# Performance work log

Hardware: AMD Instinct MI355X
Metric: run time of the kernel (lower is better)

## Reference

```python
import jax, jax.numpy as jnp
import numpy as np

N_NODES = 50000
N_NEIB = 64
D = 256
BATCH = 1024
N_SAMPLES = (25, 10)  # fanout per layer (layer_specs n_sample)


def setup_inputs() -> dict:
    key = jax.random.key(0)
    ks = jax.random.split(key, 12)
    inp = {
        'ids': jax.random.randint(ks[0], (BATCH,), 0, N_NODES),
        'diff_idx': jax.random.randint(ks[1], (N_NODES, N_NEIB), 0, N_NODES),
        'diff_val': jax.random.uniform(ks[2], (N_NODES, N_NEIB), dtype=jnp.float32),
        'feats': jax.random.normal(ks[3], (N_NODES, D), dtype=jnp.float32),
    }
    # two aggregator layers, each: fc_x, fc_neib : D -> D (= output_dim//2)
    for li in range(2):
        inp[f'Wx{li+1}'] = jax.random.normal(ks[4 + 4 * li], (D, D), dtype=jnp.float32) * 0.05
        inp[f'bx{li+1}'] = jnp.zeros((D,), dtype=jnp.float32)
        inp[f'Wn{li+1}'] = jax.random.normal(ks[5 + 4 * li], (D, D), dtype=jnp.float32) * 0.05
        inp[f'bn{li+1}'] = jnp.zeros((D,), dtype=jnp.float32)
    return inp


def _sample(diff_idx, diff_val, ids, n_samples, key):
    # gather candidate neighbor rows, shared random column permutation, take first n_samples
    tmp_idx = diff_idx[ids]            # [n, N_NEIB]
    tmp_val = diff_val[ids]
    perm = jax.random.permutation(key, tmp_idx.shape[1])
    idx = tmp_idx[:, perm][:, :n_samples].reshape(-1)
    val = tmp_val[:, perm][:, :n_samples].reshape(-1)
    return idx, val


def _agg(x, neib, vals, Wx, bx, Wn, bn):
    # weighted-mean neighbor aggregation + self/neib linear combine + relu
    n = x.shape[0]
    d = neib.shape[1]
    neib = neib.reshape(n, -1, d)              # [n, s, d]
    vals = vals.reshape(n, -1)                 # [n, s]
    w = vals / (jnp.sum(vals, axis=1, keepdims=True) + 1e-10)
    m = jnp.einsum('nsd,ns->nd', neib, w)      # weighted mean of neighbors
    return jax.nn.relu(x @ Wx + bx + m @ Wn + bn)


def reference(ids, diff_idx, diff_val, feats,
              Wx1, bx1, Wn1, bn1, Wx2, bx2, Wn2, bn2):
    skey = jax.random.key(42)
    all_feats = [feats[ids]]
    all_vals = []
    cur = ids
    for li, n in enumerate(N_SAMPLES):
        cur, vals = _sample(diff_idx, diff_val, cur, n, jax.random.fold_in(skey, li))
        all_feats.append(feats[cur])
        all_vals.append(vals)
    params = [(Wx1, bx1, Wn1, bn1), (Wx2, bx2, Wn2, bn2)]
    for Wx, bx, Wn, bn in params:
        all_feats = [_agg(all_feats[k], all_feats[k + 1], all_vals[k], Wx, bx, Wn, bn)
                     for k in range(len(all_feats) - 1)]
    assert len(all_feats) == 1
    return all_feats[0]  # [BATCH, D]
```

## Files before the change

### kernel.cpp

```cpp
#include <hip/hip_runtime.h>
#include <stdint.h>
#include <stddef.h>
#include <algorithm>

#define BATCH  1024
#define S1     25
#define S2     10
#define DIM    256
#define NNEIB  64
#define L2ROWS (BATCH * S1)
#define MROWS  (BATCH + BATCH * S1)
#define KTOT   512
#define NFEAT  50000

struct Perm25 { int p[S1]; };
struct Perm10 { int p[S2]; };

typedef __attribute__((ext_vector_type(8))) short short8;
typedef __attribute__((ext_vector_type(4))) float f32x4;

static inline uint32_t rotl_(uint32_t x, int d) { return (x << d) | (x >> (32 - d)); }

static void tf2x32(uint32_t k0, uint32_t k1, uint32_t x0, uint32_t x1,
                   uint32_t* o0, uint32_t* o1) {
  const uint32_t ks0 = k0, ks1 = k1, ks2 = k0 ^ k1 ^ 0x1BD11BDAu;
  static const int R[8] = {13, 15, 26, 6, 17, 29, 16, 24};
  x0 += ks0; x1 += ks1;
  for (int g = 0; g < 5; ++g) {
    const int* rr = R + (g & 1) * 4;
    for (int i = 0; i < 4; i++) { x0 += x1; x1 = rotl_(x1, rr[i]); x1 ^= x0; }
    uint32_t a, b;
    switch (g) {
      default:
      case 0: a = ks1; b = ks2; break;
      case 1: a = ks2; b = ks0; break;
      case 2: a = ks0; b = ks1; break;
      case 3: a = ks1; b = ks2; break;
      case 4: a = ks2; b = ks0; break;
    }
    x0 += a; x1 = x1 + b + (uint32_t)(g + 1);
  }
  *o0 = x0; *o1 = x1;
}

static void compute_perm(uint32_t li, int n, int* out) {
  uint32_t k0, k1, s0, s1;
  tf2x32(0u, 42u, 0u, li, &k0, &k1);
  tf2x32(k0, k1, 0u, 1u, &s0, &s1);
  uint32_t bits[NNEIB];
  for (int i = 0; i < NNEIB; i++) {
    uint32_t a, b;
    tf2x32(s0, s1, 0u, (uint32_t)i, &a, &b);
    bits[i] = a ^ b;
  }
  int idx[NNEIB];
  for (int i = 0; i < NNEIB; i++) idx[i] = i;
  std::stable_sort(idx, idx + NNEIB, [&](int A, int B) { return bits[A] < bits[B]; });
  for (int j = 0; j < n; j++) out[j] = idx[j];
}

__device__ __forceinline__ unsigned short f2bf(float x) {
  union { float f; uint32_t u; } v; v.f = x;
  uint32_t r = (v.u + 0x7FFFu + ((v.u >> 16) & 1u)) >> 16;
  return (unsigned short)r;
}
__device__ __forceinline__ float bfbits2f(uint32_t lo16) {
  union { uint32_t u; float f; } v; v.u = lo16 << 16;
  return v.f;
}


#define PREP_CONVF   12500
#define PREP_CONVW   512
#define PREP_BLOCKS  (PREP_CONVF + 2 * PREP_CONVW + 4)
__global__ __launch_bounds__(256) void prep_k(
    const float* __restrict__ feats, uint32_t* __restrict__ fb,
    const float* __restrict__ Wx1, const float* __restrict__ Wn1,
    unsigned short* __restrict__ Wt1,
    const float* __restrict__ Wx2, const float* __restrict__ Wn2,
    unsigned short* __restrict__ Wt2,
    const int* __restrict__ ids, const int* __restrict__ dix,
    const float* __restrict__ dval, int* __restrict__ idx1,
    float* __restrict__ w1, Perm25 pm) {
  int b = blockIdx.x, t = threadIdx.x;
  if (b < PREP_CONVF) {
    int i = b * 256 + t;
    f32x4 v = *(const f32x4*)&feats[(size_t)i * 4];
    fb[(size_t)i * 2]     = f2bf(v.x) | ((uint32_t)f2bf(v.y) << 16);
    fb[(size_t)i * 2 + 1] = f2bf(v.z) | ((uint32_t)f2bf(v.w) << 16);
  } else if (b < PREP_CONVF + 2 * PREP_CONVW) {
    int wi = b - PREP_CONVF;
    const float* Wx = (wi < PREP_CONVW) ? Wx1 : Wx2;
    const float* Wn = (wi < PREP_CONVW) ? Wn1 : Wn2;
    unsigned short* Wt = (wi < PREP_CONVW) ? Wt1 : Wt2;
    int idx = (wi % PREP_CONVW) * 256 + t;
    int n = idx >> 9, k = idx & 511;
    float v = (k < DIM) ? Wx[(size_t)k * DIM + n] : Wn[(size_t)(k - DIM) * DIM + n];
    Wt[(size_t)n * KTOT + k] = f2bf(v);
  } else {
    int i = (b - PREP_CONVF - 2 * PREP_CONVW) * 256 + t;
    if (i >= BATCH) return;
    int nid = ids[i];
    const float* vr = dval + (size_t)nid * NNEIB;
    const int* ir = dix + (size_t)nid * NNEIB;
    float v[S1];
    float s = 0.f;
    for (int j = 0; j < S1; j++) { v[j] = vr[pm.p[j]]; s += v[j]; }
    float inv = 1.f / (s + 1e-10f);
    for (int j = 0; j < S1; j++) {
      w1[i * S1 + j] = v[j] * inv;
      idx1[i * S1 + j] = ir[pm.p[j]];
    }
  }
}

__global__ __launch_bounds__(256) void stage1_k(
    const uint2* __restrict__ fb, const int* __restrict__ idx1,
    const float* __restrict__ w1, const int* __restrict__ dix,
    const float* __restrict__ dval, Perm10 pm2, uint2* __restrict__ M1) {
  int wave = threadIdx.x >> 6, lane = threadIdx.x & 63;
  int r = blockIdx.x * 4 + wave;
  int s, nbl = 0;
  float wl = 0.f;
  if (r < BATCH) {
    s = S1;
    if (lane < S1) { nbl = idx1[r * S1 + lane]; wl = w1[r * S1 + lane]; }
  } else {
    s = S2;
    int nx = idx1[r - BATCH];
    float vj = 0.f;
    if (lane < S2) {
      int c = pm2.p[lane];
      nbl = dix[(size_t)nx * NNEIB + c];
      vj = dval[(size_t)nx * NNEIB + c];
    }
    float tot = 0.f;
    for (int j = 0; j < S2; j++) tot += __shfl(vj, j);
    wl = vj / (tot + 1e-10f);
  }
  float a0 = 0.f, a1 = 0.f, a2 = 0.f, a3 = 0.f;
  for (int j = 0; j < s; j++) {
    int nid = __shfl(nbl, j);
    float wj = __shfl(wl, j);
    uint2 u = fb[(size_t)nid * 64 + lane];
    a0 += wj * bfbits2f(u.x & 0xffffu);
    a1 += wj * bfbits2f(u.x >> 16);
    a2 += wj * bfbits2f(u.y & 0xffffu);
    a3 += wj * bfbits2f(u.y >> 16);
  }
  uint2 o;
  o.x = f2bf(a0) | ((uint32_t)f2bf(a1) << 16);
  o.y = f2bf(a2) | ((uint32_t)f2bf(a3) << 16);
  M1[(size_t)r * 64 + lane] = o;
}

__global__ __launch_bounds__(256) void stage2_k(
    const uint2* __restrict__ Hb, const float* __restrict__ w1,
    uint2* __restrict__ M2) {
  int wave = threadIdx.x >> 6, lane = threadIdx.x & 63;
  int i = blockIdx.x * 4 + wave;
  float wl = (lane < S1) ? w1[(size_t)i * S1 + lane] : 0.f;
  const uint2* hb = Hb + (size_t)(BATCH + i * S1) * 64 + lane;
  float a0 = 0.f, a1 = 0.f, a2 = 0.f, a3 = 0.f;
  for (int j = 0; j < S1; j++) {
    float wj = __shfl(wl, j);
    uint2 u = hb[(size_t)j * 64];
    a0 += wj * bfbits2f(u.x & 0xffffu);
    a1 += wj * bfbits2f(u.x >> 16);
    a2 += wj * bfbits2f(u.y & 0xffffu);
    a3 += wj * bfbits2f(u.y >> 16);
  }
  uint2 o;
  o.x = f2bf(a0) | ((uint32_t)f2bf(a1) << 16);
  o.y = f2bf(a2) | ((uint32_t)f2bf(a3) << 16);
  M2[(size_t)i * 64 + lane] = o;
}

#define BK 32
#define LPAD 40
template <int TBM, int TBN, bool OUT_BF16>
__global__ __launch_bounds__(256) void gemm_k(
    const unsigned short* __restrict__ Xsrc, const int* __restrict__ ids,
    const int* __restrict__ idx1, const unsigned short* __restrict__ Mh,
    const unsigned short* __restrict__ Wt, const float* __restrict__ bx,
    const float* __restrict__ bn, void* __restrict__ OutP) {
  constexpr int MI = TBM / 32;
  constexpr int NJ = TBN / 32;
  __shared__ __align__(16) unsigned short As[TBM][LPAD];
  __shared__ __align__(16) unsigned short Bs[TBN][LPAD];
  int t = threadIdx.x;
  int wave = t >> 6, lane = t & 63, quad = lane >> 4, l16 = lane & 15;
  int wm = (wave >> 1) * (TBM / 2);
  int wn = (wave & 1) * (TBN / 2);
  int row0 = blockIdx.x * TBM, col0 = blockIdx.y * TBN;

  f32x4 acc[MI][NJ];
#pragma unroll
  for (int i = 0; i < MI; i++)
#pragma unroll
    for (int j = 0; j < NJ; j++) acc[i][j] = (f32x4){0.f, 0.f, 0.f, 0.f};

  int lr = t >> 2;
  int lq = (t & 3) * 8;
  int xrow[TBM / 64];
#pragma unroll
  for (int p = 0; p < TBM / 64; p++) {
    int gr = row0 + p * 64 + lr;
    xrow[p] = ids ? ((gr < BATCH) ? ids[gr] : idx1[gr - BATCH]) : gr;
  }

  for (int k0 = 0; k0 < KTOT; k0 += BK) {
#pragma unroll
    for (int p = 0; p < TBM / 64; p++) {
      const unsigned short* src =
          (k0 < DIM) ? (Xsrc + (size_t)xrow[p] * DIM + k0 + lq)
                     : (Mh + (size_t)(row0 + p * 64 + lr) * DIM + (k0 - DIM) + lq);
      *(f32x4*)&As[p * 64 + lr][lq] = *(const f32x4*)src;
    }
#pragma unroll
    for (int p = 0; p < TBN / 64; p++)
      *(f32x4*)&Bs[p * 64 + lr][lq] =
          *(const f32x4*)&Wt[(size_t)(col0 + p * 64 + lr) * KTOT + k0 + lq];
    __syncthreads();

    short8 af[MI], bfr[NJ];
#pragma unroll
    for (int i = 0; i < MI; i++)
      af[i] = *(const short8*)&As[wm + i * 16 + l16][quad * 8];
#pragma unroll
    for (int j = 0; j < NJ; j++)
      bfr[j] = *(const short8*)&Bs[wn + j * 16 + l16][quad * 8];
#pragma unroll
    for (int i = 0; i < MI; i++)
#pragma unroll
      for (int j = 0; j < NJ; j++)
        acc[i][j] = __builtin_amdgcn_mfma_f32_16x16x32_bf16(af[i], bfr[j], acc[i][j], 0, 0, 0);
    __syncthreads();
  }

  float bias[NJ];
#pragma unroll
  for (int j = 0; j < NJ; j++) {
    int c = col0 + wn + j * 16 + l16;
    bias[j] = bx[c] + bn[c];
  }
#pragma unroll
  for (int i = 0; i < MI; i++) {
#pragma unroll
    for (int j = 0; j < NJ; j++) {
      int c = col0 + wn + j * 16 + l16;
#pragma unroll
      for (int reg = 0; reg < 4; reg++) {
        int r = row0 + wm + i * 16 + quad * 4 + reg;
        float v = fmaxf(acc[i][j][reg] + bias[j], 0.f);
        if (OUT_BF16)
          ((unsigned short*)OutP)[(size_t)r * DIM + c] = f2bf(v);
        else
          ((float*)OutP)[(size_t)r * DIM + c] = v;
      }
    }
  }
}

static inline size_t align256(size_t x) { return (x + 255) & ~(size_t)255; }

extern "C" void kernel_launch(void* const* d_in, const int* in_sizes, int n_in,
                              void* d_out, int out_size, void* d_ws, size_t ws_size,
                              hipStream_t stream) {
  const int*   ids  = (const int*)d_in[0];
  const int*   dix  = (const int*)d_in[1];
  const float* dval = (const float*)d_in[2];
  const float* feats= (const float*)d_in[3];
  const float* Wx1  = (const float*)d_in[4];
  const float* bx1  = (const float*)d_in[5];
  const float* Wn1  = (const float*)d_in[6];
  const float* bn1  = (const float*)d_in[7];
  const float* Wx2  = (const float*)d_in[8];
  const float* bx2  = (const float*)d_in[9];
  const float* Wn2  = (const float*)d_in[10];
  const float* bn2  = (const float*)d_in[11];
  float* out = (float*)d_out;

  Perm25 p25;
  Perm10 p10;
  compute_perm(0u, S1, p25.p);
  compute_perm(1u, S2, p10.p);

  char* w = (char*)d_ws;
  int*            idx1 = (int*)w;            w += align256(sizeof(int) * L2ROWS);
  float*          w1   = (float*)w;          w += align256(sizeof(float) * L2ROWS);
  uint32_t*       fb   = (uint32_t*)w;       w += align256(2 * (size_t)NFEAT * DIM);
  unsigned short* M1   = (unsigned short*)w; w += align256(2 * (size_t)MROWS * DIM);
  unsigned short* Hb   = (unsigned short*)w; w += align256(2 * (size_t)MROWS * DIM);
  unsigned short* M2   = (unsigned short*)w; w += align256(2 * (size_t)BATCH * DIM);
  unsigned short* Wt1  = (unsigned short*)w; w += align256(2 * (size_t)DIM * KTOT);
  unsigned short* Wt2  = (unsigned short*)w; w += align256(2 * (size_t)DIM * KTOT);

  prep_k<<<PREP_BLOCKS, 256, 0, stream>>>(feats, fb, Wx1, Wn1, Wt1, Wx2, Wn2, Wt2,
                                          ids, dix, dval, idx1, w1, p25);
  stage1_k<<<MROWS / 4, 256, 0, stream>>>((const uint2*)fb, idx1, w1, dix, dval, p10,
                                          (uint2*)M1);
  gemm_k<128, 128, true><<<dim3(MROWS / 128, DIM / 128), 256, 0, stream>>>(
      (const unsigned short*)fb, ids, idx1, M1, Wt1, bx1, bn1, Hb);
  stage2_k<<<BATCH / 4, 256, 0, stream>>>((const uint2*)Hb, w1, (uint2*)M2);
  gemm_k<64, 64, false><<<dim3(BATCH / 64, DIM / 64), 256, 0, stream>>>(
      Hb, nullptr, nullptr, M2, Wt2, bx2, bn2, out);
}
```

Before: 186.3 us.

## Build contiguous concatenated GEMM operands and load tiles via global_load_lds

The aggregation kernels now write a concatenated [self | neighbor-mean] bf16 row of width 512 per output row, so the GEMM reads one contiguous A matrix instead of gathering self features through ids/idx1 indirection. The GEMM tile loads switch to direct global-to-LDS 16-byte loads, with the LDS padding removed, so data bypasses registers. The aggregation loops are also fully unrolled. In exchange, the stage kernels write extra bytes (the self half), and the unpadded LDS layout may cause bank conflicts on the MFMA fragment reads.

```diff
diff --git a/kernel.cpp b/kernel.cpp
--- a/kernel.cpp
+++ b/kernel.cpp
@@ -68,6 +68,11 @@
   union { uint32_t u; float f; } v; v.u = lo16 << 16;
   return v.f;
 }
+__device__ __forceinline__ void gload16(const unsigned short* g, unsigned short* l) {
+  __builtin_amdgcn_global_load_lds(
+      (const __attribute__((address_space(1))) unsigned int*)g,
+      (__attribute__((address_space(3))) unsigned int*)l, 16, 0, 0);
+}
 
 
 #define PREP_CONVF   12500
@@ -86,8 +91,10 @@
   if (b < PREP_CONVF) {
     int i = b * 256 + t;
     f32x4 v = *(const f32x4*)&feats[(size_t)i * 4];
-    fb[(size_t)i * 2]     = f2bf(v.x) | ((uint32_t)f2bf(v.y) << 16);
-    fb[(size_t)i * 2 + 1] = f2bf(v.z) | ((uint32_t)f2bf(v.w) << 16);
+    uint2 o;
+    o.x = f2bf(v.x) | ((uint32_t)f2bf(v.y) << 16);
+    o.y = f2bf(v.z) | ((uint32_t)f2bf(v.w) << 16);
+    ((uint2*)fb)[i] = o;
   } else if (b < PREP_CONVF + 2 * PREP_CONVW) {
     int wi = b - PREP_CONVF;
     const float* Wx = (wi < PREP_CONVW) ? Wx1 : Wx2;
@@ -115,53 +122,69 @@
 }
 
 __global__ __launch_bounds__(256) void stage1_k(
-    const uint2* __restrict__ fb, const int* __restrict__ idx1,
-    const float* __restrict__ w1, const int* __restrict__ dix,
-    const float* __restrict__ dval, Perm10 pm2, uint2* __restrict__ M1) {
+    const uint2* __restrict__ fb, const int* __restrict__ ids,
+    const int* __restrict__ idx1, const float* __restrict__ w1,
+    const int* __restrict__ dix, const float* __restrict__ dval, Perm10 pm2,
+    uint2* __restrict__ A1) {
   int wave = threadIdx.x >> 6, lane = threadIdx.x & 63;
   int r = blockIdx.x * 4 + wave;
-  int s, nbl = 0;
-  float wl = 0.f;
+  float a0 = 0.f, a1 = 0.f, a2 = 0.f, a3 = 0.f;
+  int xr;
   if (r < BATCH) {
-    s = S1;
+    xr = ids[r];
+    int nbl = 0; float wl = 0.f;
     if (lane < S1) { nbl = idx1[r * S1 + lane]; wl = w1[r * S1 + lane]; }
+#pragma unroll
+    for (int j = 0; j < S1; j++) {
+      int nid = __shfl(nbl, j);
+      float wj = __shfl(wl, j);
+      uint2 u = fb[(size_t)nid * 64 + lane];
+      a0 += wj * bfbits2f(u.x & 0xffffu);
+      a1 += wj * bfbits2f(u.x >> 16);
+      a2 += wj * bfbits2f(u.y & 0xffffu);
+      a3 += wj * bfbits2f(u.y >> 16);
+    }
   } else {
-    s = S2;
     int nx = idx1[r - BATCH];
-    float vj = 0.f;
+    xr = nx;
+    int nbl = 0; float vj = 0.f;
     if (lane < S2) {
       int c = pm2.p[lane];
       nbl = dix[(size_t)nx * NNEIB + c];
       vj = dval[(size_t)nx * NNEIB + c];
     }
     float tot = 0.f;
+#pragma unroll
     for (int j = 0; j < S2; j++) tot += __shfl(vj, j);
-    wl = vj / (tot + 1e-10f);
-  }
-  float a0 = 0.f, a1 = 0.f, a2 = 0.f, a3 = 0.f;
-  for (int j = 0; j < s; j++) {
-    int nid = __shfl(nbl, j);
-    float wj = __shfl(wl, j);
-    uint2 u = fb[(size_t)nid * 64 + lane];
-    a0 += wj * bfbits2f(u.x & 0xffffu);
-    a1 += wj * bfbits2f(u.x >> 16);
-    a2 += wj * bfbits2f(u.y & 0xffffu);
-    a3 += wj * bfbits2f(u.y >> 16);
-  }
+    float wl = vj / (tot + 1e-10f);
+#pragma unroll
+    for (int j = 0; j < S2; j++) {
+      int nid = __shfl(nbl, j);
+      float wj = __shfl(wl, j);
+      uint2 u = fb[(size_t)nid * 64 + lane];
+      a0 += wj * bfbits2f(u.x & 0xffffu);
+      a1 += wj * bfbits2f(u.x >> 16);
+      a2 += wj * bfbits2f(u.y & 0xffffu);
+      a3 += wj * bfbits2f(u.y >> 16);
+    }
+  }
+  uint2 xv = fb[(size_t)xr * 64 + lane];
   uint2 o;
   o.x = f2bf(a0) | ((uint32_t)f2bf(a1) << 16);
   o.y = f2bf(a2) | ((uint32_t)f2bf(a3) << 16);
-  M1[(size_t)r * 64 + lane] = o;
+  A1[(size_t)r * 128 + lane] = xv;
+  A1[(size_t)r * 128 + 64 + lane] = o;
 }
 
 __global__ __launch_bounds__(256) void stage2_k(
     const uint2* __restrict__ Hb, const float* __restrict__ w1,
-    uint2* __restrict__ M2) {
+    uint2* __restrict__ A2) {
   int wave = threadIdx.x >> 6, lane = threadIdx.x & 63;
   int i = blockIdx.x * 4 + wave;
   float wl = (lane < S1) ? w1[(size_t)i * S1 + lane] : 0.f;
   const uint2* hb = Hb + (size_t)(BATCH + i * S1) * 64 + lane;
   float a0 = 0.f, a1 = 0.f, a2 = 0.f, a3 = 0.f;
+#pragma unroll
   for (int j = 0; j < S1; j++) {
     float wj = __shfl(wl, j);
     uint2 u = hb[(size_t)j * 64];
@@ -170,24 +193,24 @@
     a2 += wj * bfbits2f(u.y & 0xffffu);
     a3 += wj * bfbits2f(u.y >> 16);
   }
+  uint2 xv = Hb[(size_t)i * 64 + lane];
   uint2 o;
   o.x = f2bf(a0) | ((uint32_t)f2bf(a1) << 16);
   o.y = f2bf(a2) | ((uint32_t)f2bf(a3) << 16);
-  M2[(size_t)i * 64 + lane] = o;
+  A2[(size_t)i * 128 + lane] = xv;
+  A2[(size_t)i * 128 + 64 + lane] = o;
 }
 
 #define BK 32
-#define LPAD 40
 template <int TBM, int TBN, bool OUT_BF16>
 __global__ __launch_bounds__(256) void gemm_k(
-    const unsigned short* __restrict__ Xsrc, const int* __restrict__ ids,
-    const int* __restrict__ idx1, const unsigned short* __restrict__ Mh,
-    const unsigned short* __restrict__ Wt, const float* __restrict__ bx,
-    const float* __restrict__ bn, void* __restrict__ OutP) {
+    const unsigned short* __restrict__ A, const unsigned short* __restrict__ Wt,
+    const float* __restrict__ bx, const float* __restrict__ bn,
+    void* __restrict__ OutP) {
   constexpr int MI = TBM / 32;
   constexpr int NJ = TBN / 32;
-  __shared__ __align__(16) unsigned short As[TBM][LPAD];
-  __shared__ __align__(16) unsigned short Bs[TBN][LPAD];
+  __shared__ __align__(16) unsigned short As[TBM][BK];
+  __shared__ __align__(16) unsigned short Bs[TBN][BK];
   int t = threadIdx.x;
   int wave = t >> 6, lane = t & 63, quad = lane >> 4, l16 = lane & 15;
   int wm = (wave >> 1) * (TBM / 2);
@@ -200,27 +223,20 @@
 #pragma unroll
     for (int j = 0; j < NJ; j++) acc[i][j] = (f32x4){0.f, 0.f, 0.f, 0.f};
 
-  int lr = t >> 2;
-  int lq = (t & 3) * 8;
-  int xrow[TBM / 64];
-#pragma unroll
-  for (int p = 0; p < TBM / 64; p++) {
-    int gr = row0 + p * 64 + lr;
-    xrow[p] = ids ? ((gr < BATCH) ? ids[gr] : idx1[gr - BATCH]) : gr;
-  }
+  int rl = lane >> 2;
+  int cl = (lane & 3) * 8;
 
   for (int k0 = 0; k0 < KTOT; k0 += BK) {
 #pragma unroll
-    for (int p = 0; p < TBM / 64; p++) {
-      const unsigned short* src =
-          (k0 < DIM) ? (Xsrc + (size_t)xrow[p] * DIM + k0 + lq)
-                     : (Mh + (size_t)(row0 + p * 64 + lr) * DIM + (k0 - DIM) + lq);
-      *(f32x4*)&As[p * 64 + lr][lq] = *(const f32x4*)src;
-    }
-#pragma unroll
-    for (int p = 0; p < TBN / 64; p++)
-      *(f32x4*)&Bs[p * 64 + lr][lq] =
-          *(const f32x4*)&Wt[(size_t)(col0 + p * 64 + lr) * KTOT + k0 + lq];
+    for (int c = 0; c < TBM / 64; c++) {
+      int row = c * 64 + wave * 16 + rl;
+      gload16(A + (size_t)(row0 + row) * KTOT + k0 + cl, &As[c * 64 + wave * 16][0]);
+    }
+#pragma unroll
+    for (int c = 0; c < TBN / 64; c++) {
+      int row = c * 64 + wave * 16 + rl;
+      gload16(Wt + (size_t)(col0 + row) * KTOT + k0 + cl, &Bs[c * 64 + wave * 16][0]);
+    }
     __syncthreads();
 
     short8 af[MI], bfr[NJ];
@@ -290,19 +306,19 @@
   int*            idx1 = (int*)w;            w += align256(sizeof(int) * L2ROWS);
   float*          w1   = (float*)w;          w += align256(sizeof(float) * L2ROWS);
   uint32_t*       fb   = (uint32_t*)w;       w += align256(2 * (size_t)NFEAT * DIM);
-  unsigned short* M1   = (unsigned short*)w; w += align256(2 * (size_t)MROWS * DIM);
+  unsigned short* A1   = (unsigned short*)w; w += align256(2 * (size_t)MROWS * KTOT);
   unsigned short* Hb   = (unsigned short*)w; w += align256(2 * (size_t)MROWS * DIM);
-  unsigned short* M2   = (unsigned short*)w; w += align256(2 * (size_t)BATCH * DIM);
+  unsigned short* A2   = (unsigned short*)w; w += align256(2 * (size_t)BATCH * KTOT);
   unsigned short* Wt1  = (unsigned short*)w; w += align256(2 * (size_t)DIM * KTOT);
   unsigned short* Wt2  = (unsigned short*)w; w += align256(2 * (size_t)DIM * KTOT);
 
   prep_k<<<PREP_BLOCKS, 256, 0, stream>>>(feats, fb, Wx1, Wn1, Wt1, Wx2, Wn2, Wt2,
                                           ids, dix, dval, idx1, w1, p25);
-  stage1_k<<<MROWS / 4, 256, 0, stream>>>((const uint2*)fb, idx1, w1, dix, dval, p10,
-                                          (uint2*)M1);
+  stage1_k<<<MROWS / 4, 256, 0, stream>>>((const uint2*)fb, ids, idx1, w1, dix, dval,
+                                          p10, (uint2*)A1);
   gemm_k<128, 128, true><<<dim3(MROWS / 128, DIM / 128), 256, 0, stream>>>(
-      (const unsigned short*)fb, ids, idx1, M1, Wt1, bx1, bn1, Hb);
-  stage2_k<<<BATCH / 4, 256, 0, stream>>>((const uint2*)Hb, w1, (uint2*)M2);
+      A1, Wt1, bx1, bn1, Hb);
+  stage2_k<<<BATCH / 4, 256, 0, stream>>>((const uint2*)Hb, w1, (uint2*)A2);
   gemm_k<64, 64, false><<<dim3(BATCH / 64, DIM / 64), 256, 0, stream>>>(
-      Hb, nullptr, nullptr, M2, Wt2, bx2, bn2, out);
-}
+      A2, Wt2, bx2, bn2, out);
+}
```

Result: no change. 182.9 us (-1.8%).
